# Kernel optimization log

Measured on AMD Instinct MI355X. Metric: run time of the kernel, lower is better.

## Reference

```python
import jax, jax.numpy as jnp
import numpy as np

DEP_NUM, HEAD_NUM, BSZ, DIM, REL = 96, 96, 16, 512, 128


def setup_inputs() -> dict:
    key = jax.random.key(0)
    k1, k2, k3, k4 = jax.random.split(key, 4)
    outs = jax.random.normal(k1, (DEP_NUM, BSZ, DIM), dtype=jnp.float32)
    graph_state = jax.random.normal(k2, (HEAD_NUM, BSZ, DIM), dtype=jnp.float32)
    # nn.init.normal_(std=0.02) for both weights, zero biases
    Wt = 0.02 * jax.random.normal(k3, (DIM, 2 * DIM), dtype=jnp.float32)
    bt = jnp.zeros((DIM,), dtype=jnp.float32)
    Wp = 0.02 * jax.random.normal(k4, (REL, DIM), dtype=jnp.float32)
    bp = jnp.zeros((REL,), dtype=jnp.float32)
    return {"outs": outs, "graph_state": graph_state, "Wt": Wt, "bt": bt, "Wp": Wp, "bp": bp}


def reference(outs, graph_state, Wt, bt, Wp, bp):
    # outs: [dep, b, D], graph_state: [head, b, D]
    # Linear(cat(dep, head)) == dep @ Wt[:, :D].T + head @ Wt[:, D:].T + bt
    D = outs.shape[-1]
    dep_proj = jnp.einsum('dbi,ei->dbe', outs, Wt[:, :D])           # [dep, b, D]
    head_proj = jnp.einsum('hbi,ei->hbe', graph_state, Wt[:, D:])   # [head, b, D]
    # broadcast-sum to pairwise: [dep, b, head, D]
    h = jax.nn.relu(dep_proj[:, :, None, :] + jnp.swapaxes(head_proj, 0, 1)[None] + bt)
    # dropout: identity in eval mode
    scores = jnp.einsum('dbhe,re->dbhr', h, Wp) + bp                # [dep, b, head, REL]
    nil = jnp.zeros(scores.shape[:-1] + (1,), dtype=scores.dtype)
    scores = jnp.concatenate([nil, scores], axis=-1)                # [dep, b, head, REL+1]
    return jax.nn.log_softmax(scores, axis=-1)
```

## Files before the change

### kernel.cpp

```cpp
#include <hip/hip_runtime.h>
#include <math.h>

#define DEP   96
#define HEADS 96
#define BSZ   16
#define DIM   512
#define REL   128
#define RELP  129

typedef __attribute__((ext_vector_type(8))) _Float16  half8;
typedef __attribute__((ext_vector_type(2))) __fp16    fp16x2;
typedef __attribute__((ext_vector_type(4))) float     floatx4;

__device__ __forceinline__ unsigned short f2h(float x) {
    union { _Float16 h; unsigned short u; } c;
    c.h = (_Float16)x;
    return c.u;
}
__device__ __forceinline__ unsigned pk_f2h(float a, float b) {
    union { fp16x2 h; unsigned u; } c;
    c.h = __builtin_amdgcn_cvt_pkrtz(a, b);
    return c.u;
}
__device__ __forceinline__ unsigned pk_add_h2(unsigned a, unsigned b) {
    unsigned r; asm("v_pk_add_f16 %0, %1, %2" : "=v"(r) : "v"(a), "v"(b)); return r;
}
__device__ __forceinline__ unsigned pk_max_h2(unsigned a, unsigned b) {
    unsigned r; asm("v_pk_max_f16 %0, %1, %2" : "=v"(r) : "v"(a), "v"(b)); return r;
}

#define PSS 72

__global__ __launch_bounds__(256) void proj_kernel(
    const float* __restrict__ outs, const float* __restrict__ graph,
    const float* __restrict__ Wt, const float* __restrict__ bt,
    const float* __restrict__ Wp,
    float* __restrict__ P1, unsigned short* __restrict__ P2H,
    unsigned short* __restrict__ WpF)
{
    {
        const int fb = (blockIdx.z * gridDim.y + blockIdx.y) * gridDim.x + blockIdx.x;
        if (fb < 32) {
            const int c    = fb * 256 + (int)threadIdx.x;
            const int ln   = c & 63;
            const int nq   = (c >> 6) & 7;
            const int kk   = c >> 9;
            const int row  = (nq >> 2) * 64 + (nq & 3) * 16 + (ln & 15);
            const int col  = kk * 32 + ((ln >> 4) & 3) * 8;
            const float* src = Wp + (size_t)row * DIM + col;
            float4 a = *(const float4*)src;
            float4 b = *(const float4*)(src + 4);
            uint4 o;
            o.x = pk_f2h(a.x, a.y); o.y = pk_f2h(a.z, a.w);
            o.z = pk_f2h(b.x, b.y); o.w = pk_f2h(b.z, b.w);
            *(uint4*)(WpF + (size_t)c * 8) = o;
        }
    }

    const int z = blockIdx.z;
    const float* A = z ? graph : outs;
    const int off  = z ? DIM : 0;
    const int row0 = blockIdx.y * 32;
    const int col0 = blockIdx.x * 64;

    __shared__ __align__(16) unsigned short As[32 * PSS];
    __shared__ __align__(16) unsigned short Ws[64 * PSS];

    const int tid  = threadIdx.x;
    const int lane = tid & 63;
    const int wv   = tid >> 6;
    const int ln15 = lane & 15;
    const int quad = lane >> 4;
    const int mh   = wv & 1;
    const int nh   = wv >> 1;

    floatx4 acc[2];
    acc[0] = (floatx4){0.f,0.f,0.f,0.f};
    acc[1] = (floatx4){0.f,0.f,0.f,0.f};

    for (int kt = 0; kt < DIM; kt += 64) {
        {
            const int r  = tid >> 3;
            const int e8 = (tid & 7) * 8;
            const float* p = A + (size_t)(row0 + r) * DIM + kt + e8;
            float4 va = *(const float4*)p;
            float4 vb = *(const float4*)(p + 4);
            uint4 o;
            o.x = pk_f2h(va.x, va.y); o.y = pk_f2h(va.z, va.w);
            o.z = pk_f2h(vb.x, vb.y); o.w = pk_f2h(vb.z, vb.w);
            *(uint4*)&As[r * PSS + e8] = o;
        }
        #pragma unroll
        for (int q = 0; q < 2; ++q) {
            const int slot = q*256 + tid;
            const int r  = slot >> 3;
            const int e8 = (slot & 7) * 8;
            const float* p = Wt + (size_t)(col0 + r) * (2*DIM) + off + kt + e8;
            float4 va = *(const float4*)p;
            float4 vb = *(const float4*)(p + 4);
            uint4 o;
            o.x = pk_f2h(va.x, va.y); o.y = pk_f2h(va.z, va.w);
            o.z = pk_f2h(vb.x, vb.y); o.w = pk_f2h(vb.z, vb.w);
            *(uint4*)&Ws[r * PSS + e8] = o;
        }
        __syncthreads();
        #pragma unroll
        for (int ks = 0; ks < 64; ks += 32) {
            half8 af = *(const half8*)&As[(mh*16 + ln15) * PSS + ks + quad*8];
            #pragma unroll
            for (int nt = 0; nt < 2; ++nt) {
                half8 bf8 = *(const half8*)&Ws[(nh*32 + nt*16 + ln15) * PSS + ks + quad*8];
                acc[nt] = __builtin_amdgcn_mfma_f32_16x16x32_f16(af, bf8, acc[nt], 0, 0, 0);
            }
        }
        __syncthreads();
    }

    #pragma unroll
    for (int nt = 0; nt < 2; ++nt) {
        #pragma unroll
        for (int reg = 0; reg < 4; ++reg) {
            const int m = row0 + mh*16 + quad*4 + reg;
            const int n = col0 + nh*32 + nt*16 + ln15;
            float v = acc[nt][reg];
            if (!z) P1[(size_t)m * DIM + n] = v + bt[n];
            else    P2H[(size_t)m * DIM + n] = f2h(v);
        }
    }
}

#define HSS 72

__global__ __launch_bounds__(256, 4) void fused_kernel(
    const float* __restrict__ P1, const unsigned short* __restrict__ P2H,
    const unsigned short* __restrict__ WpF, const float* __restrict__ bp,
    float* __restrict__ out)
{
    const int db = blockIdx.x;
    const int b  = db & 15;

    __shared__ __align__(16) unsigned short hs[96 * HSS];
    __shared__ __align__(16) unsigned short drowH[DIM];
    __shared__ float pmx[96][2];
    __shared__ float pl [96][2];
    __shared__ float lseS[96];

    const int tid  = threadIdx.x;
    const int lane = tid & 63;
    const int wv   = tid >> 6;
    const int ln15 = lane & 15;
    const int quad = lane >> 4;
    const int mh   = wv & 1;
    const int nh   = wv >> 1;
    const int e8   = (tid & 7) * 8;

    {
        float2 v = *(const float2*)(P1 + (size_t)db * DIM + tid*2);
        *(unsigned*)&drowH[tid*2] = pk_f2h(v.x, v.y);
    }
    __syncthreads();

    floatx4 acc[3][4];
    #pragma unroll
    for (int i = 0; i < 3; ++i)
        #pragma unroll
        for (int j = 0; j < 4; ++j) acc[i][j] = (floatx4){0.f,0.f,0.f,0.f};

    for (int kti = 0; kti < 8; ++kti) {
        const int kt = kti * 64;

        half8 bf[2][4];
        #pragma unroll
        for (int ks = 0; ks < 2; ++ks)
            #pragma unroll
            for (int nt = 0; nt < 4; ++nt)
                bf[ks][nt] = *(const half8*)(WpF +
                    (size_t)((((kti*2 + ks)*8 + nh*4 + nt)*64 + lane)) * 8);

        uint4 dv = *(const uint4*)&drowH[kt + e8];
        #pragma unroll
        for (int q = 0; q < 3; ++q) {
            const int h = (q*256 + tid) >> 3;
            uint4 pv = *(const uint4*)(P2H + ((size_t)h * BSZ + b) * DIM + kt + e8);
            uint4 o;
            o.x = pk_max_h2(pk_add_h2(pv.x, dv.x), 0u);
            o.y = pk_max_h2(pk_add_h2(pv.y, dv.y), 0u);
            o.z = pk_max_h2(pk_add_h2(pv.z, dv.z), 0u);
            o.w = pk_max_h2(pk_add_h2(pv.w, dv.w), 0u);
            *(uint4*)&hs[h * HSS + e8] = o;
        }
        __syncthreads();

        #pragma unroll
        for (int ks = 0; ks < 2; ++ks) {
            half8 af[3];
            #pragma unroll
            for (int mt = 0; mt < 3; ++mt)
                af[mt] = *(const half8*)&hs[(mh*48 + mt*16 + ln15) * HSS + ks*32 + quad*8];
            #pragma unroll
            for (int nt = 0; nt < 4; ++nt)
                #pragma unroll
                for (int mt = 0; mt < 3; ++mt)
                    acc[mt][nt] = __builtin_amdgcn_mfma_f32_16x16x32_f16(
                        af[mt], bf[ks][nt], acc[mt][nt], 0, 0, 0);
        }
        __syncthreads();
    }

    float bpv[4];
    #pragma unroll
    for (int nt = 0; nt < 4; ++nt) bpv[nt] = bp[nh*64 + nt*16 + ln15];

    #pragma unroll
    for (int mt = 0; mt < 3; ++mt) {
        #pragma unroll
        for (int reg = 0; reg < 4; ++reg) {
            const int m = mh*48 + mt*16 + quad*4 + reg;
            float s[4];
            #pragma unroll
            for (int nt = 0; nt < 4; ++nt) s[nt] = acc[mt][nt][reg] + bpv[nt];
            float mx = fmaxf(fmaxf(s[0], s[1]), fmaxf(s[2], s[3]));
            #pragma unroll
            for (int msk = 1; msk < 16; msk <<= 1) mx = fmaxf(mx, __shfl_xor(mx, msk));
            float l = 0.f;
            #pragma unroll
            for (int nt = 0; nt < 4; ++nt) l += __expf(s[nt] - mx);
            #pragma unroll
            for (int msk = 1; msk < 16; msk <<= 1) l += __shfl_xor(l, msk);
            if (ln15 == 0) { pmx[m][nh] = mx; pl[m][nh] = l; }
        }
    }
    __syncthreads();

    if (tid < 96) {
        const float mx0 = pmx[tid][0], mx1 = pmx[tid][1];
        const float MX = fmaxf(fmaxf(mx0, mx1), 0.f);
        const float L  = pl[tid][0] * __expf(mx0 - MX) + pl[tid][1] * __expf(mx1 - MX)
                       + __expf(-MX);
        lseS[tid] = MX + __logf(L);
    }
    __syncthreads();

    #pragma unroll
    for (int mt = 0; mt < 3; ++mt) {
        #pragma unroll
        for (int reg = 0; reg < 4; ++reg) {
            const int m = mh*48 + mt*16 + quad*4 + reg;
            const float lse = lseS[m];
            const size_t base = ((size_t)db * HEADS + m) * RELP;
            #pragma unroll
            for (int nt = 0; nt < 4; ++nt)
                out[base + 1 + nh*64 + nt*16 + ln15] = acc[mt][nt][reg] + bpv[nt] - lse;
            if (nh == 0 && ln15 == 0) out[base] = -lse;
        }
    }
}

extern "C" void kernel_launch(void* const* d_in, const int* in_sizes, int n_in,
                              void* d_out, int out_size, void* d_ws, size_t ws_size,
                              hipStream_t stream) {
    const float* outs  = (const float*)d_in[0];
    const float* graph = (const float*)d_in[1];
    const float* Wt    = (const float*)d_in[2];
    const float* bt    = (const float*)d_in[3];
    const float* Wp    = (const float*)d_in[4];
    const float* bp    = (const float*)d_in[5];
    float* out = (float*)d_out;

    float* P1           = (float*)d_ws;
    unsigned short* P2H = (unsigned short*)(P1 + 786432);
    unsigned short* WpF = P2H + 786432;

    proj_kernel<<<dim3(DIM/64, (DEP*BSZ)/32, 2), 256, 0, stream>>>(
        outs, graph, Wt, bt, Wp, P1, P2H, WpF);
    fused_kernel<<<DEP*BSZ, 256, 0, stream>>>(P1, P2H, WpF, bp, out);
}
```

Baseline: 147.0 us.

## Double-buffer the hidden tile in LDS and prefetch next K-slice during MFMA

The fused kernel now keeps two LDS buffers for the relu(dep+head) tile. While MFMAs consume the current K slice, it loads and builds the next one, which cuts the barriers per iteration from two to one. The softmax scratch arrays are aliased into the same arena to limit LDS growth. LDS use rises from about 14.5KB to 28KB per block, which may reduce occupancy at 4 blocks per CU, and register pressure goes up.

```diff
diff --git a/kernel.cpp b/kernel.cpp
--- a/kernel.cpp
+++ b/kernel.cpp
@@ -139,11 +139,11 @@
     const int db = blockIdx.x;
     const int b  = db & 15;
 
-    __shared__ __align__(16) unsigned short hs[96 * HSS];
-    __shared__ __align__(16) unsigned short drowH[DIM];
-    __shared__ float pmx[96][2];
-    __shared__ float pl [96][2];
-    __shared__ float lseS[96];
+    __shared__ __align__(16) char arena[28672];
+    unsigned short* drowH = (unsigned short*)(arena + 27648);
+    float* pmx  = (float*)arena;
+    float* pl   = pmx + 192;
+    float* lseS = pl + 192;
 
     const int tid  = threadIdx.x;
     const int lane = tid & 63;
@@ -153,6 +153,7 @@
     const int mh   = wv & 1;
     const int nh   = wv >> 1;
     const int e8   = (tid & 7) * 8;
+    const int hrow = tid >> 3;
 
     {
         float2 v = *(const float2*)(P1 + (size_t)db * DIM + tid*2);
@@ -160,43 +161,63 @@
     }
     __syncthreads();
 
-    floatx4 acc[3][4];
-    #pragma unroll
-    for (int i = 0; i < 3; ++i)
-        #pragma unroll
-        for (int j = 0; j < 4; ++j) acc[i][j] = (floatx4){0.f,0.f,0.f,0.f};
-
-    for (int kti = 0; kti < 8; ++kti) {
-        const int kt = kti * 64;
-
-        half8 bf[2][4];
-        #pragma unroll
-        for (int ks = 0; ks < 2; ++ks)
-            #pragma unroll
-            for (int nt = 0; nt < 4; ++nt)
-                bf[ks][nt] = *(const half8*)(WpF +
-                    (size_t)((((kti*2 + ks)*8 + nh*4 + nt)*64 + lane)) * 8);
-
-        uint4 dv = *(const uint4*)&drowH[kt + e8];
+    {
+        uint4 dv = *(const uint4*)&drowH[e8];
+        unsigned short* hs0 = (unsigned short*)arena;
         #pragma unroll
         for (int q = 0; q < 3; ++q) {
-            const int h = (q*256 + tid) >> 3;
-            uint4 pv = *(const uint4*)(P2H + ((size_t)h * BSZ + b) * DIM + kt + e8);
+            const int h = q*32 + hrow;
+            uint4 pv = *(const uint4*)(P2H + ((size_t)h * BSZ + b) * DIM + e8);
             uint4 o;
             o.x = pk_max_h2(pk_add_h2(pv.x, dv.x), 0u);
             o.y = pk_max_h2(pk_add_h2(pv.y, dv.y), 0u);
             o.z = pk_max_h2(pk_add_h2(pv.z, dv.z), 0u);
             o.w = pk_max_h2(pk_add_h2(pv.w, dv.w), 0u);
-            *(uint4*)&hs[h * HSS + e8] = o;
-        }
-        __syncthreads();
+            *(uint4*)&hs0[h * HSS + e8] = o;
+        }
+    }
+    __syncthreads();
+
+    floatx4 acc[3][4];
+    #pragma unroll
+    for (int i = 0; i < 3; ++i)
+        #pragma unroll
+        for (int j = 0; j < 4; ++j) acc[i][j] = (floatx4){0.f,0.f,0.f,0.f};
+
+    for (int kti = 0; kti < 8; ++kti) {
+        unsigned short* hsC = (unsigned short*)(arena + (kti & 1) * 13824);
+        unsigned short* hsN = (unsigned short*)(arena + ((kti & 1) ^ 1) * 13824);
+
+        half8 bf[2][4];
+        #pragma unroll
+        for (int ks = 0; ks < 2; ++ks)
+            #pragma unroll
+            for (int nt = 0; nt < 4; ++nt)
+                bf[ks][nt] = *(const half8*)(WpF +
+                    (size_t)((((kti*2 + ks)*8 + nh*4 + nt)*64 + lane)) * 8);
+
+        if (kti < 7) {
+            const int ktn = (kti + 1) * 64;
+            uint4 dv = *(const uint4*)&drowH[ktn + e8];
+            #pragma unroll
+            for (int q = 0; q < 3; ++q) {
+                const int h = q*32 + hrow;
+                uint4 pv = *(const uint4*)(P2H + ((size_t)h * BSZ + b) * DIM + ktn + e8);
+                uint4 o;
+                o.x = pk_max_h2(pk_add_h2(pv.x, dv.x), 0u);
+                o.y = pk_max_h2(pk_add_h2(pv.y, dv.y), 0u);
+                o.z = pk_max_h2(pk_add_h2(pv.z, dv.z), 0u);
+                o.w = pk_max_h2(pk_add_h2(pv.w, dv.w), 0u);
+                *(uint4*)&hsN[h * HSS + e8] = o;
+            }
+        }
 
         #pragma unroll
         for (int ks = 0; ks < 2; ++ks) {
             half8 af[3];
             #pragma unroll
             for (int mt = 0; mt < 3; ++mt)
-                af[mt] = *(const half8*)&hs[(mh*48 + mt*16 + ln15) * HSS + ks*32 + quad*8];
+                af[mt] = *(const half8*)&hsC[(mh*48 + mt*16 + ln15) * HSS + ks*32 + quad*8];
             #pragma unroll
             for (int nt = 0; nt < 4; ++nt)
                 #pragma unroll
@@ -204,6 +225,7 @@
                     acc[mt][nt] = __builtin_amdgcn_mfma_f32_16x16x32_f16(
                         af[mt], bf[ks][nt], acc[mt][nt], 0, 0, 0);
         }
+
         __syncthreads();
     }
 
@@ -227,15 +249,15 @@
             for (int nt = 0; nt < 4; ++nt) l += __expf(s[nt] - mx);
             #pragma unroll
             for (int msk = 1; msk < 16; msk <<= 1) l += __shfl_xor(l, msk);
-            if (ln15 == 0) { pmx[m][nh] = mx; pl[m][nh] = l; }
+            if (ln15 == 0) { pmx[m*2 + nh] = mx; pl[m*2 + nh] = l; }
         }
     }
     __syncthreads();
 
     if (tid < 96) {
-        const float mx0 = pmx[tid][0], mx1 = pmx[tid][1];
+        const float mx0 = pmx[tid*2], mx1 = pmx[tid*2 + 1];
         const float MX = fmaxf(fmaxf(mx0, mx1), 0.f);
-        const float L  = pl[tid][0] * __expf(mx0 - MX) + pl[tid][1] * __expf(mx1 - MX)
+        const float L  = pl[tid*2] * __expf(mx0 - MX) + pl[tid*2 + 1] * __expf(mx1 - MX)
                        + __expf(-MX);
         lseS[tid] = MX + __logf(L);
     }
```

Result: faster. 143.2 us (-2.6%).

## Store head projection in MFMA fragment order and drop LDS staging in fused kernel

Applied to the files above, without the earlier changes.

The proj kernel now writes the fp16 head projection directly in the per-lane MFMA A-fragment layout, indexed by batch, k-slice and m-tile. The fused kernel loads these fragments straight from global memory into registers and applies the add-ReLU there. This removes the shared-memory tile and both barriers per k-step, cutting LDS traffic and synchronisation. In exchange, the proj kernel does scattered 2-byte stores, and each wave issues uncoalesced-looking fragment loads from global or L2 with less latency hiding because the k-loop is no longer unrolled.

```diff
diff --git a/kernel.cpp b/kernel.cpp
--- a/kernel.cpp
+++ b/kernel.cpp
@@ -28,6 +28,9 @@
 __device__ __forceinline__ unsigned pk_max_h2(unsigned a, unsigned b) {
     unsigned r; asm("v_pk_max_f16 %0, %1, %2" : "=v"(r) : "v"(a), "v"(b)); return r;
 }
+__device__ __forceinline__ half8 u4_to_h8(uint4 v) {
+    union { uint4 u; half8 h; } c; c.u = v; return c.h;
+}
 
 #define PSS 72
 
@@ -35,7 +38,7 @@
     const float* __restrict__ outs, const float* __restrict__ graph,
     const float* __restrict__ Wt, const float* __restrict__ bt,
     const float* __restrict__ Wp,
-    float* __restrict__ P1, unsigned short* __restrict__ P2H,
+    float* __restrict__ P1, unsigned short* __restrict__ P2F,
     unsigned short* __restrict__ WpF)
 {
     {
@@ -123,23 +126,26 @@
             const int m = row0 + mh*16 + quad*4 + reg;
             const int n = col0 + nh*32 + nt*16 + ln15;
             float v = acc[nt][reg];
-            if (!z) P1[(size_t)m * DIM + n] = v + bt[n];
-            else    P2H[(size_t)m * DIM + n] = f2h(v);
-        }
-    }
-}
-
-#define HSS 72
+            if (!z) {
+                P1[(size_t)m * DIM + n] = v + bt[n];
+            } else {
+                const int h   = m >> 4, bb = m & 15;
+                const int kk  = n >> 5, ksl = (n >> 3) & 3, e = n & 7;
+                const int mq  = h >> 4, l15 = h & 15;
+                P2F[((((size_t)bb*16 + kk)*6 + mq)*64 + l15 + ksl*16)*8 + e] = f2h(v);
+            }
+        }
+    }
+}
 
 __global__ __launch_bounds__(256, 4) void fused_kernel(
-    const float* __restrict__ P1, const unsigned short* __restrict__ P2H,
+    const float* __restrict__ P1, const unsigned short* __restrict__ P2F,
     const unsigned short* __restrict__ WpF, const float* __restrict__ bp,
     float* __restrict__ out)
 {
     const int db = blockIdx.x;
     const int b  = db & 15;
 
-    __shared__ __align__(16) unsigned short hs[96 * HSS];
     __shared__ __align__(16) unsigned short drowH[DIM];
     __shared__ float pmx[96][2];
     __shared__ float pl [96][2];
@@ -152,7 +158,6 @@
     const int quad = lane >> 4;
     const int mh   = wv & 1;
     const int nh   = wv >> 1;
-    const int e8   = (tid & 7) * 8;
 
     {
         float2 v = *(const float2*)(P1 + (size_t)db * DIM + tid*2);
@@ -166,45 +171,38 @@
         #pragma unroll
         for (int j = 0; j < 4; ++j) acc[i][j] = (floatx4){0.f,0.f,0.f,0.f};
 
+    const unsigned short* p2b = P2F + (size_t)b * (16*6*64*8);
+
+    #pragma unroll 1
     for (int kti = 0; kti < 8; ++kti) {
-        const int kt = kti * 64;
-
-        half8 bf[2][4];
-        #pragma unroll
-        for (int ks = 0; ks < 2; ++ks)
+        #pragma unroll
+        for (int ks = 0; ks < 2; ++ks) {
+            const int kk = kti*2 + ks;
+            uint4 dk = *(const uint4*)&drowH[kti*64 + ks*32 + quad*8];
+            half8 af[3];
+            #pragma unroll
+            for (int mt = 0; mt < 3; ++mt) {
+                uint4 pa = *(const uint4*)(p2b +
+                    ((size_t)(kk*6 + mh*3 + mt)*64 + lane) * 8);
+                uint4 o;
+                o.x = pk_max_h2(pk_add_h2(pa.x, dk.x), 0u);
+                o.y = pk_max_h2(pk_add_h2(pa.y, dk.y), 0u);
+                o.z = pk_max_h2(pk_add_h2(pa.z, dk.z), 0u);
+                o.w = pk_max_h2(pk_add_h2(pa.w, dk.w), 0u);
+                af[mt] = u4_to_h8(o);
+            }
+            half8 bf[4];
             #pragma unroll
             for (int nt = 0; nt < 4; ++nt)
-                bf[ks][nt] = *(const half8*)(WpF +
-                    (size_t)((((kti*2 + ks)*8 + nh*4 + nt)*64 + lane)) * 8);
-
-        uint4 dv = *(const uint4*)&drowH[kt + e8];
-        #pragma unroll
-        for (int q = 0; q < 3; ++q) {
-            const int h = (q*256 + tid) >> 3;
-            uint4 pv = *(const uint4*)(P2H + ((size_t)h * BSZ + b) * DIM + kt + e8);
-            uint4 o;
-            o.x = pk_max_h2(pk_add_h2(pv.x, dv.x), 0u);
-            o.y = pk_max_h2(pk_add_h2(pv.y, dv.y), 0u);
-            o.z = pk_max_h2(pk_add_h2(pv.z, dv.z), 0u);
-            o.w = pk_max_h2(pk_add_h2(pv.w, dv.w), 0u);
-            *(uint4*)&hs[h * HSS + e8] = o;
-        }
-        __syncthreads();
-
-        #pragma unroll
-        for (int ks = 0; ks < 2; ++ks) {
-            half8 af[3];
-            #pragma unroll
-            for (int mt = 0; mt < 3; ++mt)
-                af[mt] = *(const half8*)&hs[(mh*48 + mt*16 + ln15) * HSS + ks*32 + quad*8];
+                bf[nt] = *(const half8*)(WpF +
+                    (size_t)((kk*8 + nh*4 + nt)*64 + lane) * 8);
             #pragma unroll
             for (int nt = 0; nt < 4; ++nt)
                 #pragma unroll
                 for (int mt = 0; mt < 3; ++mt)
                     acc[mt][nt] = __builtin_amdgcn_mfma_f32_16x16x32_f16(
-                        af[mt], bf[ks][nt], acc[mt][nt], 0, 0, 0);
-        }
-        __syncthreads();
+                        af[mt], bf[nt], acc[mt][nt], 0, 0, 0);
+        }
     }
 
     float bpv[4];
@@ -268,10 +266,10 @@
     float* out = (float*)d_out;
 
     float* P1           = (float*)d_ws;
-    unsigned short* P2H = (unsigned short*)(P1 + 786432);
-    unsigned short* WpF = P2H + 786432;
+    unsigned short* P2F = (unsigned short*)(P1 + 786432);
+    unsigned short* WpF = P2F + 786432;
 
     proj_kernel<<<dim3(DIM/64, (DEP*BSZ)/32, 2), 256, 0, stream>>>(
-        outs, graph, Wt, bt, Wp, P1, P2H, WpF);
-    fused_kernel<<<DEP*BSZ, 256, 0, stream>>>(P1, P2H, WpF, bp, out);
-}
+        outs, graph, Wt, bt, Wp, P1, P2F, WpF);
+    fused_kernel<<<DEP*BSZ, 256, 0, stream>>>(P1, P2F, WpF, bp, out);
+}
```

After: 151.3 us. +2.9%, slower.
